# Kernel tuning notes

Measured on AMD Instinct MI355X. Metric: run time of the kernel, lower is better.

The kernel has to match this reference:

```python
import jax, jax.numpy as jnp
import numpy as np

# Sampled softmax loss (tf.nn.sampled_softmax_loss with log-uniform candidate
# sampler, unique=True, remove_accidental_hits=True), vectorized over the batch
# instead of the original per-example tf.map_fn.

NEG_INF = -1e9


def _log_uniform_logp(ids, num_classes):
    # P(c) = (log(c+2) - log(c+1)) / log(num_classes + 1)
    ids = ids.astype(jnp.float32)
    return jnp.log(jnp.log1p(1.0 / (ids + 1.0)) / jnp.log(num_classes + 1.0))


def _log_expected_count(ids, num_sampled, num_classes):
    # unique sampling: E[count] = 1 - (1 - p)^num_sampled  (TF's formula)
    logp = _log_uniform_logp(ids, num_classes)
    return jnp.log(-jnp.expm1(num_sampled * jnp.log1p(-jnp.exp(logp))))


def setup_inputs() -> dict:
    key = jax.random.key(0)
    k1, k2, k3, k4 = jax.random.split(key, 4)
    B, T, D = 32, 512, 1024
    N, S = 50000, 4096
    x = jax.random.normal(k1, (B, T, D), dtype=jnp.float32)
    W = jax.random.normal(k2, (N, D), dtype=jnp.float32) * 0.02
    b = jnp.zeros((N,), dtype=jnp.float32)
    labels = jax.random.randint(k3, (B, T), 0, N, dtype=jnp.int64)
    sampled = jax.random.randint(k4, (B, S), 0, N, dtype=jnp.int64)
    return {"x": x, "W": W, "b": b, "labels": labels, "sampled": sampled}


def reference(x, W, b, labels, sampled):
    N = W.shape[0]
    S = sampled.shape[-1]
    # true class logits: [B,T]
    true_w = W[labels]                                   # [B,T,D] gather
    true_logit = jnp.einsum("btd,btd->bt", x, true_w) + b[labels]
    true_logit = true_logit - _log_expected_count(labels, S, N)
    # sampled class logits: [B,T,S]
    samp_w = W[sampled]                                  # [B,S,D] gather
    samp_logits = jnp.einsum("btd,bsd->bts", x, samp_w)
    samp_logits = samp_logits + (b[sampled] - _log_expected_count(sampled, S, N))[:, None, :]
    # remove accidental hits (sampled id == true label)
    hit = sampled[:, None, :] == labels[:, :, None]      # [B,T,S]
    samp_logits = jnp.where(hit, NEG_INF, samp_logits)
    # softmax cross-entropy with the true class at index 0
    all_logits = jnp.concatenate([true_logit[..., None], samp_logits], axis=-1)
    token_loss = jax.nn.logsumexp(all_logits, axis=-1) - true_logit  # [B,T]
    per_example = jnp.mean(token_loss, axis=-1)                      # [B]
    return 0.5 * jnp.mean(per_example)
```

## Files before the change

kernel.cpp:

```cpp
#include <hip/hip_runtime.h>
#include <hip/hip_bf16.h>
#include <math.h>
#include <stdint.h>

#define B_ 32
#define T_ 512
#define D_ 1024
#define N_ 50000
#define S_ 4096

#define INV_LOG_NP1 0.09242317f

typedef __attribute__((ext_vector_type(8))) short bf16x8;
typedef __attribute__((ext_vector_type(4))) float f32x4;
typedef __attribute__((ext_vector_type(4))) short s16x4;
typedef __attribute__((ext_vector_type(8))) short s16x8;

__device__ __forceinline__ short f2bf(float f) {
    unsigned u = __float_as_uint(f);
    u += 0x7fffu + ((u >> 16) & 1u);
    return (short)(u >> 16);
}

__device__ __forceinline__ float log_expected(int id) {
    float p  = log1pf(1.0f / ((float)id + 1.0f)) * INV_LOG_NP1;
    return logf(-expm1f((float)S_ * log1pf(-p)));
}

__device__ __forceinline__ void gload_lds16(const short* g, short* l) {
    __builtin_amdgcn_global_load_lds(
        (const __attribute__((address_space(1))) void*)g,
        (__attribute__((address_space(3))) void*)l, 16, 0, 0);
}

__global__ __launch_bounds__(256) void convert_w_kernel(
    const float* __restrict__ W, short* __restrict__ Wbf)
{
    size_t i = ((size_t)blockIdx.x * 2048) + (size_t)threadIdx.x * 8;
    float4 a = *(const float4*)(W + i);
    float4 b = *(const float4*)(W + i + 4);
    s16x8 o = {f2bf(a.x), f2bf(a.y), f2bf(a.z), f2bf(a.w),
               f2bf(b.x), f2bf(b.y), f2bf(b.z), f2bf(b.w)};
    *(s16x8*)(Wbf + i) = o;
}

template <bool EMIT_XBF>
__global__ __launch_bounds__(256) void true_logit_kernel(
    const float* __restrict__ x, const float* __restrict__ W,
    const float* __restrict__ bvec, const int* __restrict__ labels,
    float* __restrict__ true_logit, float* __restrict__ denom,
    short* __restrict__ xbf)
{
    int w = threadIdx.x >> 6, lane = threadIdx.x & 63;
    int token = blockIdx.x * 4 + w;
    int lab = labels[token];
    const float4* xp = (const float4*)(x + (size_t)token * D_);
    const float4* wp = (const float4*)(W + (size_t)lab * D_);
    float acc = 0.0f;
#pragma unroll
    for (int j = 0; j < 4; ++j) {
        float4 a = xp[lane + 64 * j];
        float4 c = wp[lane + 64 * j];
        acc += a.x * c.x + a.y * c.y + a.z * c.z + a.w * c.w;
        if (EMIT_XBF) {
            s16x4 pa = {f2bf(a.x), f2bf(a.y), f2bf(a.z), f2bf(a.w)};
            *(s16x4*)(xbf + (size_t)token * D_ + (lane + 64 * j) * 4) = pa;
        }
    }
#pragma unroll
    for (int m = 32; m >= 1; m >>= 1) acc += __shfl_xor(acc, m);
    if (lane == 0) {
        float tl = acc + bvec[lab] - log_expected(lab);
        true_logit[token] = tl;
        denom[token] = __expf(tl);
    }
}

constexpr int BM = 128, BN = 128, BK = 32;

__global__ __launch_bounds__(256) void sampled_gemm_bf16(
    const short* __restrict__ xbf, const short* __restrict__ Wbf,
    const float* __restrict__ bvec, const int* __restrict__ labels,
    const int* __restrict__ sampled, float* __restrict__ denom)
{
    __shared__ short At[BM * BK];
    __shared__ short Bt[BN * BK];
    __shared__ float colbias[BN];
    __shared__ int   ids[BN];
    __shared__ int   labT[BM];

    int bidx = blockIdx.x;
    int b    = bidx >> 7;
    int rem  = bidx & 127;
    int mT   = rem >> 5;
    int nT   = rem & 31;

    int tid = threadIdx.x;

    if (tid < BN) {
        int id = sampled[b * S_ + nT * BN + tid];
        ids[tid] = id;
        colbias[tid] = bvec[id] - log_expected(id);
    } else {
        int i = tid - BN;
        labT[i] = labels[b * T_ + mT * BM + i];
    }
    __syncthreads();

    int w = tid >> 6, lane = tid & 63;
    int rl = lane >> 2;
    int c  = (lane & 3) ^ (rl & 3);

    int tokBase = b * T_ + mT * BM;
    const short* pA0 = xbf + (size_t)(tokBase + (2 * w)     * 16 + rl) * D_ + c * 8;
    const short* pA1 = xbf + (size_t)(tokBase + (2 * w + 1) * 16 + rl) * D_ + c * 8;
    const short* pB0 = Wbf + (size_t)ids[(2 * w)     * 16 + rl] * D_ + c * 8;
    const short* pB1 = Wbf + (size_t)ids[(2 * w + 1) * 16 + rl] * D_ + c * 8;
    short* lA0 = At + (2 * w) * 512;
    short* lA1 = At + (2 * w + 1) * 512;
    short* lB0 = Bt + (2 * w) * 512;
    short* lB1 = Bt + (2 * w + 1) * 512;

    f32x4 acc[4][4];
#pragma unroll
    for (int mi = 0; mi < 4; ++mi)
#pragma unroll
        for (int ni = 0; ni < 4; ++ni) acc[mi][ni] = (f32x4){0.f, 0.f, 0.f, 0.f};

    int waveM = w >> 1, waveN = w & 1;
    int lr = lane & 15, lq = lane >> 4;
    int aoff[4], boff[4];
#pragma unroll
    for (int i = 0; i < 4; ++i) {
        aoff[i] = (waveM * 64 + i * 16 + lr) * BK + ((lq ^ (lr & 3)) * 8);
        boff[i] = (waveN * 64 + i * 16 + lr) * BK + ((lq ^ (lr & 3)) * 8);
    }

    for (int k0 = 0; k0 < D_; k0 += BK) {
        __syncthreads();
        gload_lds16(pA0, lA0);
        gload_lds16(pA1, lA1);
        gload_lds16(pB0, lB0);
        gload_lds16(pB1, lB1);
        pA0 += BK; pA1 += BK; pB0 += BK; pB1 += BK;
        __syncthreads();

        bf16x8 af[4], bfr[4];
#pragma unroll
        for (int mi = 0; mi < 4; ++mi) af[mi]  = *(const bf16x8*)&At[aoff[mi]];
#pragma unroll
        for (int ni = 0; ni < 4; ++ni) bfr[ni] = *(const bf16x8*)&Bt[boff[ni]];
#pragma unroll
        for (int mi = 0; mi < 4; ++mi)
#pragma unroll
            for (int ni = 0; ni < 4; ++ni)
                acc[mi][ni] = __builtin_amdgcn_mfma_f32_16x16x32_bf16(
                    af[mi], bfr[ni], acc[mi][ni], 0, 0, 0);
    }

    float* dptr = denom + b * T_ + mT * BM;
#pragma unroll
    for (int mi = 0; mi < 4; ++mi) {
#pragma unroll
        for (int r = 0; r < 4; ++r) {
            int localRow = waveM * 64 + mi * 16 + lq * 4 + r;
            int lab = labT[localRow];
            float s = 0.0f;
#pragma unroll
            for (int ni = 0; ni < 4; ++ni) {
                int col = waveN * 64 + ni * 16 + lr;
                float v = acc[mi][ni][r] + colbias[col];
                s += (ids[col] == lab) ? 0.0f : __expf(v);
            }
            s += __shfl_xor(s, 1);
            s += __shfl_xor(s, 2);
            s += __shfl_xor(s, 4);
            s += __shfl_xor(s, 8);
            if (lr == 0) atomicAdd(&dptr[localRow], s);
        }
    }
}

__global__ __launch_bounds__(256) void sampled_gemm(
    const float* __restrict__ x, const float* __restrict__ W,
    const float* __restrict__ bvec, const int* __restrict__ labels,
    const int* __restrict__ sampled, float* __restrict__ denom)
{
    __shared__ short At[BM * BK];
    __shared__ short Bt[BN * BK];
    __shared__ float colbias[BN];
    __shared__ int   ids[BN];
    __shared__ int   labT[BM];

    int bidx = blockIdx.x;
    int b    = bidx >> 7;
    int rem  = bidx & 127;
    int mT   = rem >> 5;
    int nT   = rem & 31;
    int tid = threadIdx.x;

    if (tid < BN) {
        int id = sampled[b * S_ + nT * BN + tid];
        ids[tid] = id;
        colbias[tid] = bvec[id] - log_expected(id);
    } else {
        int i = tid - BN;
        labT[i] = labels[b * T_ + mT * BM + i];
    }
    __syncthreads();

    const float* asrc[4];
    const float* bsrc[4];
    int ch = tid & 7;
#pragma unroll
    for (int j = 0; j < 4; ++j) {
        int row = (tid >> 3) + 32 * j;
        asrc[j] = x + ((size_t)(b * T_ + mT * BM + row)) * D_ + ch * 4;
        bsrc[j] = W + (size_t)ids[row] * D_ + ch * 4;
    }

    f32x4 acc[4][4];
#pragma unroll
    for (int mi = 0; mi < 4; ++mi)
#pragma unroll
        for (int ni = 0; ni < 4; ++ni) acc[mi][ni] = (f32x4){0.f, 0.f, 0.f, 0.f};

    int w = tid >> 6, lane = tid & 63;
    int waveM = w >> 1, waveN = w & 1;
    int lr = lane & 15, lq = lane >> 4;

    for (int k0 = 0; k0 < D_; k0 += BK) {
        __syncthreads();
#pragma unroll
        for (int j = 0; j < 4; ++j) {
            int row = (tid >> 3) + 32 * j;
            float4 va = *(const float4*)(asrc[j] + k0);
            s16x4 pa = {f2bf(va.x), f2bf(va.y), f2bf(va.z), f2bf(va.w)};
            *(s16x4*)&At[row * BK + ch * 4] = pa;
            float4 vb = *(const float4*)(bsrc[j] + k0);
            s16x4 pb = {f2bf(vb.x), f2bf(vb.y), f2bf(vb.z), f2bf(vb.w)};
            *(s16x4*)&Bt[row * BK + ch * 4] = pb;
        }
        __syncthreads();
        bf16x8 af[4], bfr[4];
#pragma unroll
        for (int mi = 0; mi < 4; ++mi)
            af[mi] = *(const bf16x8*)&At[(waveM * 64 + mi * 16 + lr) * BK + lq * 8];
#pragma unroll
        for (int ni = 0; ni < 4; ++ni)
            bfr[ni] = *(const bf16x8*)&Bt[(waveN * 64 + ni * 16 + lr) * BK + lq * 8];
#pragma unroll
        for (int mi = 0; mi < 4; ++mi)
#pragma unroll
            for (int ni = 0; ni < 4; ++ni)
                acc[mi][ni] = __builtin_amdgcn_mfma_f32_16x16x32_bf16(
                    af[mi], bfr[ni], acc[mi][ni], 0, 0, 0);
    }

    float* dptr = denom + b * T_ + mT * BM;
#pragma unroll
    for (int mi = 0; mi < 4; ++mi) {
#pragma unroll
        for (int r = 0; r < 4; ++r) {
            int localRow = waveM * 64 + mi * 16 + lq * 4 + r;
            int lab = labT[localRow];
            float s = 0.0f;
#pragma unroll
            for (int ni = 0; ni < 4; ++ni) {
                int col = waveN * 64 + ni * 16 + lr;
                float v = acc[mi][ni][r] + colbias[col];
                s += (ids[col] == lab) ? 0.0f : __expf(v);
            }
            s += __shfl_xor(s, 1);
            s += __shfl_xor(s, 2);
            s += __shfl_xor(s, 4);
            s += __shfl_xor(s, 8);
            if (lr == 0) atomicAdd(&dptr[localRow], s);
        }
    }
}

__global__ __launch_bounds__(256) void finalize_kernel(
    const float* __restrict__ true_logit, const float* __restrict__ denom,
    float* __restrict__ out)
{
    float s = 0.0f;
    for (int i = threadIdx.x; i < B_ * T_; i += 256)
        s += __logf(denom[i]) - true_logit[i];
#pragma unroll
    for (int m = 32; m >= 1; m >>= 1) s += __shfl_xor(s, m);
    __shared__ float wsum[4];
    if ((threadIdx.x & 63) == 0) wsum[threadIdx.x >> 6] = s;
    __syncthreads();
    if (threadIdx.x == 0)
        out[0] = 0.5f * (wsum[0] + wsum[1] + wsum[2] + wsum[3]) / (float)(B_ * T_);
}

extern "C" void kernel_launch(void* const* d_in, const int* in_sizes, int n_in,
                              void* d_out, int out_size, void* d_ws, size_t ws_size,
                              hipStream_t stream) {
    const float* x       = (const float*)d_in[0];
    const float* W       = (const float*)d_in[1];
    const float* bvec    = (const float*)d_in[2];
    const int*   labels  = (const int*)d_in[3];
    const int*   sampled = (const int*)d_in[4];
    float* out = (float*)d_out;

    float* true_logit = (float*)d_ws;
    float* denom      = true_logit + B_ * T_;
    short* xbf        = (short*)(denom + B_ * T_);
    short* Wbf        = xbf + (size_t)B_ * T_ * D_;

    const size_t NEED = (size_t)2 * B_ * T_ * 4
                      + (size_t)B_ * T_ * D_ * 2
                      + (size_t)N_ * D_ * 2;

    if (ws_size >= NEED) {
        convert_w_kernel<<<N_ * D_ / 2048, 256, 0, stream>>>(W, Wbf);
        true_logit_kernel<true><<<B_ * T_ / 4, 256, 0, stream>>>(
            x, W, bvec, labels, true_logit, denom, xbf);
        sampled_gemm_bf16<<<B_ * (T_ / BM) * (S_ / BN), 256, 0, stream>>>(
            xbf, Wbf, bvec, labels, sampled, denom);
    } else {
        true_logit_kernel<false><<<B_ * T_ / 4, 256, 0, stream>>>(
            x, W, bvec, labels, true_logit, denom, nullptr);
        sampled_gemm<<<B_ * (T_ / BM) * (S_ / BN), 256, 0, stream>>>(
            x, W, bvec, labels, sampled, denom);
    }
    finalize_kernel<<<1, 256, 0, stream>>>(true_logit, denom, out);
}
```

Before: 583.6 us.

## Double-buffer LDS tiles in sampled GEMM and prefetch the next K slice

Splits the A and B shared-memory tiles into two buffers, so the next K slice is loaded from global memory while MFMA work runs on the current one. This removes one of the two barriers per step that the single-buffer loop needed. Sampled row ids are now read straight from global memory rather than waiting on the shared id array, so the first tile load can start before the bias setup. The LDS XOR swizzle is also changed to use (row>>1)&3 to reduce bank conflicts. Shared memory use per block doubles, which may lower occupancy.

```diff
diff --git a/kernel.cpp b/kernel.cpp
--- a/kernel.cpp
+++ b/kernel.cpp
@@ -83,8 +83,8 @@
     const float* __restrict__ bvec, const int* __restrict__ labels,
     const int* __restrict__ sampled, float* __restrict__ denom)
 {
-    __shared__ short At[BM * BK];
-    __shared__ short Bt[BN * BK];
+    __shared__ short At[2][BM * BK];
+    __shared__ short Bt[2][BN * BK];
     __shared__ float colbias[BN];
     __shared__ int   ids[BN];
     __shared__ int   labT[BM];
@@ -95,7 +95,36 @@
     int mT   = rem >> 5;
     int nT   = rem & 31;
 
-    int tid = threadIdx.x;
+    int tid  = threadIdx.x;
+    int w    = tid >> 6, lane = tid & 63;
+
+    int rl = lane >> 2;
+    int sl = lane & 3;
+    int c  = sl ^ ((rl >> 1) & 3);
+    int segA = 2 * w, segB = 2 * w + 1;
+    int tokBase = b * T_ + mT * BM;
+
+    int idr0 = sampled[b * S_ + nT * BN + segA * 16 + rl];
+    int idr1 = sampled[b * S_ + nT * BN + segB * 16 + rl];
+
+    const short* gA0 = xbf + (size_t)(tokBase + segA * 16 + rl) * D_ + c * 8;
+    const short* gA1 = xbf + (size_t)(tokBase + segB * 16 + rl) * D_ + c * 8;
+    const short* gB0 = Wbf + (size_t)idr0 * D_ + c * 8;
+    const short* gB1 = Wbf + (size_t)idr1 * D_ + c * 8;
+    short* lA0[2] = {&At[0][segA * 512], &At[1][segA * 512]};
+    short* lA1[2] = {&At[0][segB * 512], &At[1][segB * 512]};
+    short* lB0[2] = {&Bt[0][segA * 512], &Bt[1][segA * 512]};
+    short* lB1[2] = {&Bt[0][segB * 512], &Bt[1][segB * 512]};
+
+#define STAGE(buf, koff)                          \
+    do {                                          \
+        gload_lds16(gA0 + (koff), lA0[buf]);      \
+        gload_lds16(gA1 + (koff), lA1[buf]);      \
+        gload_lds16(gB0 + (koff), lB0[buf]);      \
+        gload_lds16(gB1 + (koff), lB1[buf]);      \
+    } while (0)
+
+    STAGE(0, 0);
 
     if (tid < BN) {
         int id = sampled[b * S_ + nT * BN + tid];
@@ -105,21 +134,6 @@
         int i = tid - BN;
         labT[i] = labels[b * T_ + mT * BM + i];
     }
-    __syncthreads();
-
-    int w = tid >> 6, lane = tid & 63;
-    int rl = lane >> 2;
-    int c  = (lane & 3) ^ (rl & 3);
-
-    int tokBase = b * T_ + mT * BM;
-    const short* pA0 = xbf + (size_t)(tokBase + (2 * w)     * 16 + rl) * D_ + c * 8;
-    const short* pA1 = xbf + (size_t)(tokBase + (2 * w + 1) * 16 + rl) * D_ + c * 8;
-    const short* pB0 = Wbf + (size_t)ids[(2 * w)     * 16 + rl] * D_ + c * 8;
-    const short* pB1 = Wbf + (size_t)ids[(2 * w + 1) * 16 + rl] * D_ + c * 8;
-    short* lA0 = At + (2 * w) * 512;
-    short* lA1 = At + (2 * w + 1) * 512;
-    short* lB0 = Bt + (2 * w) * 512;
-    short* lB1 = Bt + (2 * w + 1) * 512;
 
     f32x4 acc[4][4];
 #pragma unroll
@@ -129,34 +143,41 @@
 
     int waveM = w >> 1, waveN = w & 1;
     int lr = lane & 15, lq = lane >> 4;
+    int sw = lq ^ ((lr >> 1) & 3);
     int aoff[4], boff[4];
 #pragma unroll
     for (int i = 0; i < 4; ++i) {
-        aoff[i] = (waveM * 64 + i * 16 + lr) * BK + ((lq ^ (lr & 3)) * 8);
-        boff[i] = (waveN * 64 + i * 16 + lr) * BK + ((lq ^ (lr & 3)) * 8);
-    }
-
-    for (int k0 = 0; k0 < D_; k0 += BK) {
+        aoff[i] = (waveM * 64 + i * 16 + lr) * BK + sw * 8;
+        boff[i] = (waveN * 64 + i * 16 + lr) * BK + sw * 8;
+    }
+
+#define COMPUTE(buf)                                                        \
+    do {                                                                    \
+        bf16x8 af[4], bfr[4];                                               \
+        _Pragma("unroll")                                                   \
+        for (int mi = 0; mi < 4; ++mi)                                      \
+            af[mi] = *(const bf16x8*)&At[buf][aoff[mi]];                    \
+        _Pragma("unroll")                                                   \
+        for (int ni = 0; ni < 4; ++ni)                                      \
+            bfr[ni] = *(const bf16x8*)&Bt[buf][boff[ni]];                   \
+        _Pragma("unroll")                                                   \
+        for (int mi = 0; mi < 4; ++mi)                                      \
+            _Pragma("unroll")                                               \
+            for (int ni = 0; ni < 4; ++ni)                                  \
+                acc[mi][ni] = __builtin_amdgcn_mfma_f32_16x16x32_bf16(      \
+                    af[mi], bfr[ni], acc[mi][ni], 0, 0, 0);                 \
+    } while (0)
+
+    for (int k0 = 0; k0 < D_; k0 += 2 * BK) {
         __syncthreads();
-        gload_lds16(pA0, lA0);
-        gload_lds16(pA1, lA1);
-        gload_lds16(pB0, lB0);
-        gload_lds16(pB1, lB1);
-        pA0 += BK; pA1 += BK; pB0 += BK; pB1 += BK;
+        STAGE(1, k0 + BK);
+        COMPUTE(0);
         __syncthreads();
-
-        bf16x8 af[4], bfr[4];
-#pragma unroll
-        for (int mi = 0; mi < 4; ++mi) af[mi]  = *(const bf16x8*)&At[aoff[mi]];
-#pragma unroll
-        for (int ni = 0; ni < 4; ++ni) bfr[ni] = *(const bf16x8*)&Bt[boff[ni]];
-#pragma unroll
-        for (int mi = 0; mi < 4; ++mi)
-#pragma unroll
-            for (int ni = 0; ni < 4; ++ni)
-                acc[mi][ni] = __builtin_amdgcn_mfma_f32_16x16x32_bf16(
-                    af[mi], bfr[ni], acc[mi][ni], 0, 0, 0);
-    }
+        if (k0 + 2 * BK < D_) STAGE(0, k0 + 2 * BK);
+        COMPUTE(1);
+    }
+#undef STAGE
+#undef COMPUTE
 
     float* dptr = denom + b * T_ + mT * BM;
 #pragma unroll
```

New measurement: 589.7 us. About the same (+1.0%).

## Double BK to 64 in bf16 sampled GEMM and prefetch first stage before setup

Applied to the files above, without the earlier changes.

Raises the K-tile depth of the bf16 sampled GEMM from 32 to 64, halving the number of barrier pairs and global-to-LDS load rounds per block. The load mapping and LDS swizzle are reworked for 8-chunk rows, and each K tile is consumed in two MFMA sub-steps. The first tile's loads are issued before the shared bias/id setup so they overlap it, with sample ids read directly from global memory. LDS use per block doubles, which may lower occupancy. The fp32 fallback kernel keeps a fixed K-tile of 32.

```diff
diff --git a/kernel.cpp b/kernel.cpp
--- a/kernel.cpp
+++ b/kernel.cpp
@@ -76,7 +76,7 @@
     }
 }
 
-constexpr int BM = 128, BN = 128, BK = 32;
+constexpr int BM = 128, BN = 128, BK = 64;
 
 __global__ __launch_bounds__(256) void sampled_gemm_bf16(
     const short* __restrict__ xbf, const short* __restrict__ Wbf,
@@ -95,7 +95,38 @@
     int mT   = rem >> 5;
     int nT   = rem & 31;
 
-    int tid = threadIdx.x;
+    int tid  = threadIdx.x;
+    int w    = tid >> 6, lane = tid & 63;
+
+    int r = lane >> 3;
+    int s = lane & 7;
+    int c = s ^ r;
+
+    int tokBase = b * T_ + mT * BM;
+    const short* gA[4];
+    const short* gB[4];
+    short* lA[4];
+    short* lB[4];
+#pragma unroll
+    for (int j = 0; j < 4; ++j) {
+        int seg = 4 * w + j;
+        int row = seg * 8 + r;
+        gA[j] = xbf + (size_t)(tokBase + row) * D_ + c * 8;
+        int id = sampled[b * S_ + nT * BN + row];
+        gB[j] = Wbf + (size_t)id * D_ + c * 8;
+        lA[j] = At + seg * 512;
+        lB[j] = Bt + seg * 512;
+    }
+
+#define STAGE()                                                      \
+    do {                                                             \
+        _Pragma("unroll")                                            \
+        for (int j = 0; j < 4; ++j) { gload_lds16(gA[j], lA[j]); gA[j] += BK; } \
+        _Pragma("unroll")                                            \
+        for (int j = 0; j < 4; ++j) { gload_lds16(gB[j], lB[j]); gB[j] += BK; } \
+    } while (0)
+
+    STAGE();
 
     if (tid < BN) {
         int id = sampled[b * S_ + nT * BN + tid];
@@ -105,21 +136,6 @@
         int i = tid - BN;
         labT[i] = labels[b * T_ + mT * BM + i];
     }
-    __syncthreads();
-
-    int w = tid >> 6, lane = tid & 63;
-    int rl = lane >> 2;
-    int c  = (lane & 3) ^ (rl & 3);
-
-    int tokBase = b * T_ + mT * BM;
-    const short* pA0 = xbf + (size_t)(tokBase + (2 * w)     * 16 + rl) * D_ + c * 8;
-    const short* pA1 = xbf + (size_t)(tokBase + (2 * w + 1) * 16 + rl) * D_ + c * 8;
-    const short* pB0 = Wbf + (size_t)ids[(2 * w)     * 16 + rl] * D_ + c * 8;
-    const short* pB1 = Wbf + (size_t)ids[(2 * w + 1) * 16 + rl] * D_ + c * 8;
-    short* lA0 = At + (2 * w) * 512;
-    short* lA1 = At + (2 * w + 1) * 512;
-    short* lB0 = Bt + (2 * w) * 512;
-    short* lB1 = Bt + (2 * w + 1) * 512;
 
     f32x4 acc[4][4];
 #pragma unroll
@@ -129,54 +145,60 @@
 
     int waveM = w >> 1, waveN = w & 1;
     int lr = lane & 15, lq = lane >> 4;
-    int aoff[4], boff[4];
+    int aRow[4], bRow[4];
 #pragma unroll
     for (int i = 0; i < 4; ++i) {
-        aoff[i] = (waveM * 64 + i * 16 + lr) * BK + ((lq ^ (lr & 3)) * 8);
-        boff[i] = (waveN * 64 + i * 16 + lr) * BK + ((lq ^ (lr & 3)) * 8);
-    }
+        aRow[i] = (waveM * 64 + i * 16 + lr) * BK;
+        bRow[i] = (waveN * 64 + i * 16 + lr) * BK;
+    }
+    int slt[2];
+    slt[0] = ((0 + lq) ^ (lr & 7)) * 8;
+    slt[1] = ((4 + lq) ^ (lr & 7)) * 8;
 
     for (int k0 = 0; k0 < D_; k0 += BK) {
+        if (k0) {
+            __syncthreads();
+            STAGE();
+        }
         __syncthreads();
-        gload_lds16(pA0, lA0);
-        gload_lds16(pA1, lA1);
-        gload_lds16(pB0, lB0);
-        gload_lds16(pB1, lB1);
-        pA0 += BK; pA1 += BK; pB0 += BK; pB1 += BK;
-        __syncthreads();
-
-        bf16x8 af[4], bfr[4];
-#pragma unroll
-        for (int mi = 0; mi < 4; ++mi) af[mi]  = *(const bf16x8*)&At[aoff[mi]];
-#pragma unroll
-        for (int ni = 0; ni < 4; ++ni) bfr[ni] = *(const bf16x8*)&Bt[boff[ni]];
-#pragma unroll
-        for (int mi = 0; mi < 4; ++mi)
+#pragma unroll
+        for (int t = 0; t < 2; ++t) {
+            bf16x8 af[4], bfr[4];
+#pragma unroll
+            for (int mi = 0; mi < 4; ++mi)
+                af[mi] = *(const bf16x8*)&At[aRow[mi] + slt[t]];
 #pragma unroll
             for (int ni = 0; ni < 4; ++ni)
-                acc[mi][ni] = __builtin_amdgcn_mfma_f32_16x16x32_bf16(
-                    af[mi], bfr[ni], acc[mi][ni], 0, 0, 0);
-    }
+                bfr[ni] = *(const bf16x8*)&Bt[bRow[ni] + slt[t]];
+#pragma unroll
+            for (int mi = 0; mi < 4; ++mi)
+#pragma unroll
+                for (int ni = 0; ni < 4; ++ni)
+                    acc[mi][ni] = __builtin_amdgcn_mfma_f32_16x16x32_bf16(
+                        af[mi], bfr[ni], acc[mi][ni], 0, 0, 0);
+        }
+    }
+#undef STAGE
 
     float* dptr = denom + b * T_ + mT * BM;
 #pragma unroll
     for (int mi = 0; mi < 4; ++mi) {
 #pragma unroll
-        for (int r = 0; r < 4; ++r) {
-            int localRow = waveM * 64 + mi * 16 + lq * 4 + r;
+        for (int rr = 0; rr < 4; ++rr) {
+            int localRow = waveM * 64 + mi * 16 + lq * 4 + rr;
             int lab = labT[localRow];
-            float s = 0.0f;
+            float sum = 0.0f;
 #pragma unroll
             for (int ni = 0; ni < 4; ++ni) {
                 int col = waveN * 64 + ni * 16 + lr;
-                float v = acc[mi][ni][r] + colbias[col];
-                s += (ids[col] == lab) ? 0.0f : __expf(v);
+                float v = acc[mi][ni][rr] + colbias[col];
+                sum += (ids[col] == lab) ? 0.0f : __expf(v);
             }
-            s += __shfl_xor(s, 1);
-            s += __shfl_xor(s, 2);
-            s += __shfl_xor(s, 4);
-            s += __shfl_xor(s, 8);
-            if (lr == 0) atomicAdd(&dptr[localRow], s);
+            sum += __shfl_xor(sum, 1);
+            sum += __shfl_xor(sum, 2);
+            sum += __shfl_xor(sum, 4);
+            sum += __shfl_xor(sum, 8);
+            if (lr == 0) atomicAdd(&dptr[localRow], sum);
         }
     }
 }
@@ -186,8 +208,9 @@
     const float* __restrict__ bvec, const int* __restrict__ labels,
     const int* __restrict__ sampled, float* __restrict__ denom)
 {
-    __shared__ short At[BM * BK];
-    __shared__ short Bt[BN * BK];
+    constexpr int FBK = 32;
+    __shared__ short At[BM * FBK];
+    __shared__ short Bt[BN * FBK];
     __shared__ float colbias[BN];
     __shared__ int   ids[BN];
     __shared__ int   labT[BM];
@@ -229,26 +252,26 @@
     int waveM = w >> 1, waveN = w & 1;
     int lr = lane & 15, lq = lane >> 4;
 
-    for (int k0 = 0; k0 < D_; k0 += BK) {
+    for (int k0 = 0; k0 < D_; k0 += FBK) {
         __syncthreads();
 #pragma unroll
         for (int j = 0; j < 4; ++j) {
             int row = (tid >> 3) + 32 * j;
             float4 va = *(const float4*)(asrc[j] + k0);
             s16x4 pa = {f2bf(va.x), f2bf(va.y), f2bf(va.z), f2bf(va.w)};
-            *(s16x4*)&At[row * BK + ch * 4] = pa;
+            *(s16x4*)&At[row * FBK + ch * 4] = pa;
             float4 vb = *(const float4*)(bsrc[j] + k0);
             s16x4 pb = {f2bf(vb.x), f2bf(vb.y), f2bf(vb.z), f2bf(vb.w)};
-            *(s16x4*)&Bt[row * BK + ch * 4] = pb;
+            *(s16x4*)&Bt[row * FBK + ch * 4] = pb;
         }
         __syncthreads();
         bf16x8 af[4], bfr[4];
 #pragma unroll
         for (int mi = 0; mi < 4; ++mi)
-            af[mi] = *(const bf16x8*)&At[(waveM * 64 + mi * 16 + lr) * BK + lq * 8];
+            af[mi] = *(const bf16x8*)&At[(waveM * 64 + mi * 16 + lr) * FBK + lq * 8];
 #pragma unroll
         for (int ni = 0; ni < 4; ++ni)
-            bfr[ni] = *(const bf16x8*)&Bt[(waveN * 64 + ni * 16 + lr) * BK + lq * 8];
+            bfr[ni] = *(const bf16x8*)&Bt[(waveN * 64 + ni * 16 + lr) * FBK + lq * 8];
 #pragma unroll
         for (int mi = 0; mi < 4; ++mi)
 #pragma unroll
@@ -261,21 +284,21 @@
 #pragma unroll
     for (int mi = 0; mi < 4; ++mi) {
 #pragma unroll
-        for (int r = 0; r < 4; ++r) {
-            int localRow = waveM * 64 + mi * 16 + lq * 4 + r;
+        for (int rr = 0; rr < 4; ++rr) {
+            int localRow = waveM * 64 + mi * 16 + lq * 4 + rr;
             int lab = labT[localRow];
-            float s = 0.0f;
+            float sum = 0.0f;
 #pragma unroll
             for (int ni = 0; ni < 4; ++ni) {
                 int col = waveN * 64 + ni * 16 + lr;
-                float v = acc[mi][ni][r] + colbias[col];
-                s += (ids[col] == lab) ? 0.0f : __expf(v);
+                float v = acc[mi][ni][rr] + colbias[col];
+                sum += (ids[col] == lab) ? 0.0f : __expf(v);
             }
-            s += __shfl_xor(s, 1);
-            s += __shfl_xor(s, 2);
-            s += __shfl_xor(s, 4);
-            s += __shfl_xor(s, 8);
-            if (lr == 0) atomicAdd(&dptr[localRow], s);
+            sum += __shfl_xor(sum, 1);
+            sum += __shfl_xor(sum, 2);
+            sum += __shfl_xor(sum, 4);
+            sum += __shfl_xor(sum, 8);
+            if (lr == 0) atomicAdd(&dptr[localRow], sum);
         }
     }
 }
```

Result: faster. 542.7 us (-7.0%).
